# Kernel optimization log

Hardware: AMD Instinct MI355X
Metric: run time of the kernel (lower is better)

Reference implementation:

```python
import jax, jax.numpy as jnp
import numpy as np

B, S, D = 2, 2048, 2048
H, KVH, DH = 16, 4, 128
EPS = 1e-6
ROPE_BASE = 10000.0


def _rms_norm(x, eps=EPS):
    # weightless RMSNorm over the last (head) dim
    return x * jax.lax.rsqrt(jnp.mean(jnp.square(x), axis=-1, keepdims=True) + eps)


def _rope(x):
    # x: [b, s, h, d]; standard half-split RoPE, base 10000
    d = x.shape[-1]
    s = x.shape[1]
    inv_freq = 1.0 / (ROPE_BASE ** (jnp.arange(0, d // 2, dtype=jnp.float32) * 2.0 / d))
    ang = jnp.arange(s, dtype=jnp.float32)[:, None] * inv_freq[None, :]  # [s, d/2]
    cos = jnp.cos(ang)[None, :, None, :]
    sin = jnp.sin(ang)[None, :, None, :]
    x1, x2 = jnp.split(x, 2, axis=-1)
    return jnp.concatenate([x1 * cos - x2 * sin, x1 * sin + x2 * cos], axis=-1)


def setup_inputs() -> dict:
    key = jax.random.key(0)
    ks = jax.random.split(key, 5)
    x = jax.random.normal(ks[0], (B, S, D), dtype=jnp.float32)
    mask = jnp.tril(jnp.ones((S, S), dtype=bool))  # causal
    # eqx.Linear-style weights: [out, in], scaled init
    wq = jax.random.normal(ks[1], (D, D), dtype=jnp.float32) / np.sqrt(D)
    wk = jax.random.normal(ks[2], (KVH * DH, D), dtype=jnp.float32) / np.sqrt(D)
    wv = jax.random.normal(ks[3], (KVH * DH, D), dtype=jnp.float32) / np.sqrt(D)
    wo = jax.random.normal(ks[4], (D, D), dtype=jnp.float32) / np.sqrt(D)
    return {"x": x, "mask": mask, "wq": wq, "wk": wk, "wv": wv, "wo": wo}


def reference(x, mask, wq, wk, wv, wo):
    b, s, _ = x.shape
    q = jnp.einsum('bsi,oi->bso', x, wq).reshape(b, s, H, DH)
    k = jnp.einsum('bsi,oi->bso', x, wk).reshape(b, s, KVH, DH)
    v = jnp.einsum('bsi,oi->bso', x, wv).reshape(b, s, KVH, DH)
    rep = H // KVH
    k = jnp.repeat(k, rep, axis=-2)  # [b, s, H, DH]
    v = jnp.repeat(v, rep, axis=-2)
    q = _rms_norm(q)
    k = _rms_norm(k)
    q = _rope(q)
    k = _rope(k)
    scores = jnp.einsum('bshd,bthd->bhst', q, k) / jnp.sqrt(jnp.float32(DH))
    scores = jnp.where(mask[None, None], scores, -jnp.inf)
    w = jax.nn.softmax(scores, axis=-1)
    out = jnp.einsum('bhst,bthd->bshd', w, v).reshape(b, s, D)
    return jnp.einsum('bsi,oi->bso', out, wo)
```

## Files before the change

### kernel.cpp

```cpp
#include <hip/hip_runtime.h>
#include <hip/hip_bf16.h>

typedef unsigned short u16;
typedef unsigned int   u32;
typedef unsigned long long u64;
typedef __attribute__((ext_vector_type(8))) short bf16x8;
typedef __attribute__((ext_vector_type(4))) float f32x4;
typedef __attribute__((ext_vector_type(16))) float f32x16;

#define MFMA16(a,b,c) __builtin_amdgcn_mfma_f32_16x16x32_bf16((a),(b),(c),0,0,0)
#define MFMA32(a,b,c) __builtin_amdgcn_mfma_f32_32x32x16_bf16((a),(b),(c),0,0,0)

#define GLD16(gp, lp) __builtin_amdgcn_global_load_lds( \
    (const __attribute__((address_space(1))) void*)(gp), \
    (__attribute__((address_space(3))) void*)(lp), 16, 0, 0)

__device__ inline u32 pkbf(float a, float b) {
  __hip_bfloat16 ha = __float2bfloat16(a), hb = __float2bfloat16(b);
  return (u32)(*(u16*)&ha) | ((u32)(*(u16*)&hb) << 16);
}
__device__ inline float b2f(u16 x) {
  __hip_bfloat16 h; *(u16*)&h = x; return __bfloat162float(h);
}
__device__ inline u32 pk2(float a, float b) {
  u32 ua = __builtin_bit_cast(u32, a) + 0x8000u;
  u32 ub = __builtin_bit_cast(u32, b) + 0x8000u;
  return __builtin_amdgcn_perm(ub, ua, 0x07060302u);
}
__device__ inline float fmax3(float a, float b, float c) {
  return fmaxf(fmaxf(a, b), c);
}

__global__ __launch_bounds__(256) void cast_f32_bf16(const float* __restrict__ src,
                                                     u16* __restrict__ dst, int n4) {
  int i = blockIdx.x * 256 + threadIdx.x;
  if (i >= n4) return;
  float4 v = reinterpret_cast<const float4*>(src)[i];
  uint2 pk; pk.x = pkbf(v.x, v.y); pk.y = pkbf(v.z, v.w);
  reinterpret_cast<uint2*>(dst)[i] = pk;
}

__device__ inline void cstore(u16* C, size_t i, float v) {
  __hip_bfloat16 h = __float2bfloat16(v); C[i] = *(u16*)&h;
}
__device__ inline void cstore(float* C, size_t i, float v) { C[i] = v; }

template<typename OutT>
__global__ __launch_bounds__(512, 4) void gemm_big(const u16* __restrict__ A,
                                                   const u16* __restrict__ B,
                                                   OutT* __restrict__ C,
                                                   int M, int N, int K) {
  __shared__ u16 As[2][128 * 32];
  __shared__ u16 Bs[2][256 * 32];

  const int t = threadIdx.x;
  const int lane = t & 63, wid = t >> 6;
  const int l15 = lane & 15, l4 = lane >> 4;
  const int wr = wid >> 2, wc = wid & 3;

  const int nwg = gridDim.x * gridDim.y;
  int lid = blockIdx.y * gridDim.x + blockIdx.x;
  lid = (lid & 7) * (nwg >> 3) + (lid >> 3);
  const int m0 = (lid / gridDim.x) * 128, n0 = (lid % gridDim.x) * 256;

  const int ra = t >> 2;
  const int ca = (t & 3) ^ ((ra >> 1) & 3);
  const u16* Ag  = A + (size_t)(m0 + ra) * K + ca * 8;
  const u16* Bg0 = B + (size_t)(n0 + ra) * K + ca * 8;
  const u16* Bg1 = B + (size_t)(n0 + 128 + ra) * K + ca * 8;

#define STAGE(k0_, buf_) do {                                                 \
    GLD16(Ag  + (k0_), &As[buf_][t * 8]);                                     \
    GLD16(Bg0 + (k0_), &Bs[buf_][t * 8]);                                     \
    GLD16(Bg1 + (k0_), &Bs[buf_][4096 + t * 8]);                              \
  } while (0)

  const int nk = K >> 5;
  const int ks = (l15 >> 1) & 3;
  const int coff = ((l4 ^ ks) << 3);

  f32x4 acc[4][4] = {};

  STAGE(0, 0);
  STAGE(32, 1);

  for (int j = 0; j < nk; ++j) {
    const int cur = j & 1;
    if (j + 1 < nk) asm volatile("s_waitcnt vmcnt(3)" ::: "memory");
    else            asm volatile("s_waitcnt vmcnt(0)" ::: "memory");
    __builtin_amdgcn_s_barrier();
    __builtin_amdgcn_sched_barrier(0);

    bf16x8 af[4], bfr[4];
#pragma unroll
    for (int mi = 0; mi < 4; ++mi)
      af[mi] = *(const bf16x8*)&As[cur][(wr * 64 + mi * 16 + l15) * 32 + coff];
#pragma unroll
    for (int ni = 0; ni < 4; ++ni)
      bfr[ni] = *(const bf16x8*)&Bs[cur][(wc * 64 + ni * 16 + l15) * 32 + coff];
    __builtin_amdgcn_s_setprio(1);
#pragma unroll
    for (int mi = 0; mi < 4; ++mi)
#pragma unroll
      for (int ni = 0; ni < 4; ++ni)
        acc[mi][ni] = MFMA16(af[mi], bfr[ni], acc[mi][ni]);
    __builtin_amdgcn_s_setprio(0);

    __builtin_amdgcn_s_barrier();
    if (j + 2 < nk) STAGE((j + 2) << 5, cur);
  }

  const int crow = m0 + wr * 64 + (l4 << 2);
  const int ccol = n0 + wc * 64 + l15;
#pragma unroll
  for (int mi = 0; mi < 4; ++mi)
#pragma unroll
    for (int ni = 0; ni < 4; ++ni)
#pragma unroll
      for (int r = 0; r < 4; ++r)
        cstore(C, (size_t)(crow + mi * 16 + r) * N + (ccol + ni * 16), acc[mi][ni][r]);
#undef STAGE
}

__global__ __launch_bounds__(256) void rmsrope_kernel(u16* __restrict__ qkv) {
  const int t = threadIdx.x;
  const int lane = t & 63;
  const int gw = blockIdx.x * 4 + (t >> 6);
  const int row = gw / 20;
  const int hd = gw - row * 20;
  const int col = (hd < 16) ? hd * 128 : 2048 + (hd - 16) * 128;
  const size_t base = (size_t)row * 3072 + col;
  float x1 = b2f(qkv[base + lane]);
  float x2 = b2f(qkv[base + 64 + lane]);
  float ss = x1 * x1 + x2 * x2;
#pragma unroll
  for (int off = 32; off >= 1; off >>= 1) ss += __shfl_xor(ss, off, 64);
  const float qsc = (hd < 16) ? (0.08838834764831845f * 1.44269504088896340f)
                              : 1.0f;
  const float sc = rsqrtf(ss * (1.0f / 128.0f) + 1e-6f) * qsc;
  const int pos = row & 2047;
  const float inv_freq = exp2f(-(float)lane * (13.287712379549449f / 64.0f));
  float sn, cs;
  sincosf((float)pos * inv_freq, &sn, &cs);
  const float a = x1 * sc, b2 = x2 * sc;
  __hip_bfloat16 o1 = __float2bfloat16(a * cs - b2 * sn);
  __hip_bfloat16 o2 = __float2bfloat16(a * sn + b2 * cs);
  qkv[base + lane] = *(u16*)&o1;
  qkv[base + 64 + lane] = *(u16*)&o2;
}

__global__ __launch_bounds__(256) void vtrans_kernel(const u16* __restrict__ qkv,
                                                     u16* __restrict__ vt) {
  __shared__ u16 Ls[64 * 130];
  const int t = threadIdx.x;
  const int g = blockIdx.x & 7, sb = blockIdx.x >> 3;
  const int b = g >> 2, kvh = g & 3;
  const int vcol = 2560 + kvh * 128;
  {
    const int row = t >> 4, dch = t & 15;
    const u16* src = qkv + (size_t)(b * 2048 + sb * 64 + row) * 3072 + vcol + dch * 8;
#pragma unroll
    for (int it = 0; it < 4; ++it) {
      bf16x8 v = *(const bf16x8*)(src + (size_t)it * 16 * 3072);
      *(bf16x8*)&Ls[(row + it * 16) * 130 + dch * 8] = v;
    }
  }
  __syncthreads();
  const int c = t & 7, d0 = t >> 3;
  const int k0 = 4 * (8 * (c >> 2) + 4 * ((c >> 1) & 1) + (c & 1));
#pragma unroll
  for (int it = 0; it < 4; ++it) {
    const int d = d0 + 32 * it;
    u16 v[8];
#pragma unroll
    for (int e = 0; e < 8; ++e)
      v[e] = Ls[(k0 + (e & 3) + 8 * (e >> 2)) * 130 + d];
    u64 lo = (u64)v[0] | ((u64)v[1] << 16) | ((u64)v[2] << 32) | ((u64)v[3] << 48);
    u64 hi = (u64)v[4] | ((u64)v[5] << 16) | ((u64)v[6] << 32) | ((u64)v[7] << 48);
    u64* dst = (u64*)(vt + ((size_t)g * 128 + d) * 2048 + sb * 64 + c * 8);
    dst[0] = lo; dst[1] = hi;
  }
}

__global__ __launch_bounds__(256, 2) void attn_kernel(const u16* __restrict__ qkv,
                                                      const u16* __restrict__ vt,
                                                      u16* __restrict__ ao) {
  __shared__ u16 Ks[2][64 * 128];
  __shared__ u16 Vt[2][128 * 64];

  const int t = threadIdx.x;
  const int lane = t & 63, w = t >> 6;
  const int l31 = lane & 31, hi = lane >> 5;
  const int qg = w >> 1, hi2 = w & 1;

  const int bid = blockIdx.x;
  const int g = bid & 7;
  const int b = g >> 2, kvh = g & 3;
  const int idx = bid >> 3;
  const int h = kvh * 4 + (idx & 3);
  const int j = idx >> 2;

  const int kcol = 2048 + kvh * 128;
  const u16* vtg = vt + (size_t)g * 128 * 2048;

  const int krow_s = t >> 4, kchk = t & 15;
  const int vd = t >> 3, vc = t & 7;

#define STAGE_K(kb_, buf_) do {                                               \
    const size_t rb_ = (size_t)(b * 2048 + (kb_) * 64);                       \
    _Pragma("unroll")                                                         \
    for (int j_ = 0; j_ < 4; ++j_) {                                          \
      const int row_ = j_ * 16 + krow_s;                                      \
      GLD16(qkv + (rb_ + row_) * 3072 + kcol + ((kchk ^ (row_ & 7)) << 3),    \
            &Ks[buf_][(j_ * 256 + t) << 3]);                                  \
    } } while (0)

#define STAGE_V(kb_, buf_) do {                                               \
    _Pragma("unroll")                                                         \
    for (int j_ = 0; j_ < 4; ++j_) {                                          \
      const int d_ = j_ * 32 + vd;                                            \
      GLD16(vtg + (size_t)d_ * 2048 + (kb_) * 64 + ((vc ^ (d_ & 7)) << 3),    \
            &Vt[buf_][(j_ * 256 + t) << 3]);                                  \
    } } while (0)

  for (int ph = 0; ph < 2; ++ph) {
    const int qt64 = ph ? (31 - j) : j;
    const int q0 = qt64 * 64;
    const int nt = qt64 + 1;
    const int qrow = q0 + 32 * qg + l31;

    bf16x8 qf[8];
    {
      const u16* qp = qkv + (size_t)(b * 2048 + qrow) * 3072 + h * 128 + hi * 8;
#pragma unroll
      for (int st = 0; st < 8; ++st) qf[st] = *(const bf16x8*)(qp + st * 16);
    }

    f32x16 o[4];
#pragma unroll
    for (int dt = 0; dt < 4; ++dt)
#pragma unroll
      for (int i = 0; i < 16; ++i) o[dt][i] = 0.f;
    float m2 = -1e30f, l = 0.f;

    STAGE_K(0, 0);
    STAGE_V(0, 0);

    for (int kb = 0; kb < nt; ++kb) {
      const int cur = kb & 1;
      __syncthreads();
      const bool have_next = (kb + 1 < nt);
      if (have_next) {
        STAGE_K(kb + 1, cur ^ 1);
        STAGE_V(kb + 1, cur ^ 1);
      }

      f32x16 s;
#pragma unroll
      for (int i = 0; i < 16; ++i) s[i] = 0.f;
      const int kbase = (32 * hi2 + l31) * 128;
      const int ksw = l31 & 7;
      __builtin_amdgcn_s_setprio(1);
#pragma unroll
      for (int st = 0; st < 8; ++st) {
        bf16x8 ka = *(const bf16x8*)&Ks[cur][kbase + (((2 * st + hi) ^ ksw) << 3)];
        s = MFMA32(ka, qf[st], s);
      }
      __builtin_amdgcn_s_setprio(0);

      const bool nomask = (kb < qt64) || (hi2 == 0 && qg == 1);
      if (!nomask) {
#pragma unroll
        for (int i = 0; i < 16; ++i) {
          const int kr = kb * 64 + 32 * hi2 + (i & 3) + 8 * (i >> 2) + 4 * hi;
          s[i] = (kr <= qrow) ? s[i] : -INFINITY;
        }
      }
      float a0 = fmax3(s[0], s[1], s[2]);
      float a1 = fmax3(s[3], s[4], s[5]);
      float a2 = fmax3(s[6], s[7], s[8]);
      float a3 = fmax3(s[9], s[10], s[11]);
      float a4 = fmax3(s[12], s[13], s[14]);
      float b0 = fmax3(a0, a1, s[15]);
      float b1 = fmax3(a2, a3, a4);
      float pm = fmaxf(b0, b1);
      pm = fmaxf(pm, __shfl_xor(pm, 32));
      if (!__all(pm <= m2 + 8.f)) {
        const float m2n = fmaxf(m2, pm);
        const float fc = exp2f(m2 - m2n);
        m2 = m2n; l *= fc;
#pragma unroll
        for (int dt = 0; dt < 4; ++dt)
#pragma unroll
          for (int i = 0; i < 16; ++i) o[dt][i] *= fc;
      }
#pragma unroll
      for (int i = 0; i < 16; ++i) s[i] = exp2f(s[i] - m2);
      float t8[8];
#pragma unroll
      for (int i = 0; i < 8; ++i) t8[i] = s[i] + s[i + 8];
#pragma unroll
      for (int i = 0; i < 4; ++i) t8[i] = t8[i] + t8[i + 4];
      l += (t8[0] + t8[1]) + (t8[2] + t8[3]);
      union PB { u32 wd[4]; bf16x8 v; } p0u, p1u;
#pragma unroll
      for (int q_ = 0; q_ < 4; ++q_) {
        p0u.wd[q_] = pk2(s[2 * q_],     s[2 * q_ + 1]);
        p1u.wd[q_] = pk2(s[8 + 2 * q_], s[8 + 2 * q_ + 1]);
      }
      __builtin_amdgcn_s_setprio(1);
#pragma unroll
      for (int dt = 0; dt < 4; ++dt) {
        const int vrow = (dt * 32 + l31) * 64;
        const int dsw = l31 & 7;
        bf16x8 va0 = *(const bf16x8*)&Vt[cur][vrow + (((4 * hi2 + hi) ^ dsw) << 3)];
        o[dt] = MFMA32(va0, p0u.v, o[dt]);
        bf16x8 va1 = *(const bf16x8*)&Vt[cur][vrow + (((4 * hi2 + 2 + hi) ^ dsw) << 3)];
        o[dt] = MFMA32(va1, p1u.v, o[dt]);
      }
      __builtin_amdgcn_s_setprio(0);
    }

    __syncthreads();
    const float l_tot = l + __shfl_xor(l, 32);
    float* Mrg = (float*)&Ks[0][0];
    float* Mlb = (float*)&Vt[0][0];
    const int sw8 = l31 & 7;
    if (hi2) {
#pragma unroll
      for (int dt = 0; dt < 4; ++dt) {
        const int rbase = ((qg * 4 + dt) * 32 + l31) * 32;
#pragma unroll
        for (int m_ = 0; m_ < 4; ++m_) {
          f32x4 cv;
          cv[0] = o[dt][4 * m_ + 0]; cv[1] = o[dt][4 * m_ + 1];
          cv[2] = o[dt][4 * m_ + 2]; cv[3] = o[dt][4 * m_ + 3];
          *(f32x4*)&Mrg[rbase + (((hi * 4 + m_) ^ sw8) << 2)] = cv;
        }
      }
      if (hi == 0) {
        Mlb[qg * 64 + l31] = m2;
        Mlb[qg * 64 + 32 + l31] = l_tot;
      }
    }
    __syncthreads();
    if (!hi2) {
      const float m1 = Mlb[qg * 64 + l31];
      const float l1 = Mlb[qg * 64 + 32 + l31];
      const float ms = fmaxf(m2, m1);
      const float w0 = exp2f(m2 - ms), w1 = exp2f(m1 - ms);
      const float inv = 1.f / (w0 * l_tot + w1 * l1);
      const float aw0 = w0 * inv, aw1 = w1 * inv;
      const size_t orow = (size_t)(b * 2048 + qrow) * 2048 + h * 128;
#pragma unroll
      for (int dt = 0; dt < 4; ++dt) {
        const int rbase = ((qg * 4 + dt) * 32 + l31) * 32;
#pragma unroll
        for (int m_ = 0; m_ < 4; ++m_) {
          f32x4 o1v = *(const f32x4*)&Mrg[rbase + (((hi * 4 + m_) ^ sw8) << 2)];
          u64 val = 0;
#pragma unroll
          for (int r = 0; r < 4; ++r) {
            __hip_bfloat16 hb =
                __float2bfloat16(aw0 * o[dt][4 * m_ + r] + aw1 * o1v[r]);
            val |= (u64)(*(u16*)&hb) << (16 * r);
          }
          *(u64*)&ao[orow + dt * 32 + 8 * m_ + 4 * hi] = val;
        }
      }
    }
    __syncthreads();
  }
#undef STAGE_K
#undef STAGE_V
}

extern "C" void kernel_launch(void* const* d_in, const int* in_sizes, int n_in,
                              void* d_out, int out_size, void* d_ws, size_t ws_size,
                              hipStream_t stream) {
  const float* x  = (const float*)d_in[0];
  const float* wq = (const float*)d_in[2];
  const float* wk = (const float*)d_in[3];
  const float* wv = (const float*)d_in[4];
  const float* wo = (const float*)d_in[5];
  float* out = (float*)d_out;

  u16* xb   = (u16*)d_ws;
  u16* wqkv = xb + (size_t)8388608;
  u16* qkv  = wqkv + (size_t)6291456;
  u16* vtg  = qkv + (size_t)12582912;
  u16* ao   = xb;
  u16* wob  = wqkv;

  cast_f32_bf16<<<8192, 256, 0, stream>>>(x,  xb,   2097152);
  cast_f32_bf16<<<4096, 256, 0, stream>>>(wq, wqkv, 1048576);
  cast_f32_bf16<<<1024, 256, 0, stream>>>(wk, wqkv + (size_t)4194304, 262144);
  cast_f32_bf16<<<1024, 256, 0, stream>>>(wv, wqkv + (size_t)5242880, 262144);

  gemm_big<u16><<<dim3(12, 32), 512, 0, stream>>>(xb, wqkv, qkv, 4096, 3072, 2048);

  cast_f32_bf16<<<4096, 256, 0, stream>>>(wo, wob, 1048576);

  rmsrope_kernel<<<20480, 256, 0, stream>>>(qkv);
  vtrans_kernel<<<256, 256, 0, stream>>>(qkv, vtg);

  attn_kernel<<<512, 256, 0, stream>>>(qkv, vtg, ao);

  gemm_big<float><<<dim3(8, 32), 512, 0, stream>>>(ao, wob, out, 4096, 2048, 2048);
}
```

Baseline: 219.8 us.

## Enlarge attention query tile to 128 rows with 8 waves per block

Each attention block now handles 128 query rows with 512 threads instead of 64 rows with 256 threads, so every staged K/V tile in shared memory is reused by twice as many query rows. The launch grid is halved, causal pairing moves to 128-row tiles, and the mask test is recomputed per wave. Shared memory becomes one flat buffer sized for the larger merge scratch. The launch bound asks for more waves per execution unit, which halves the register budget and could cause spills. With only 256 blocks, parallelism per CU is also lower.

```diff
diff --git a/kernel.cpp b/kernel.cpp
--- a/kernel.cpp
+++ b/kernel.cpp
@@ -182,11 +182,12 @@
   }
 }
 
-__global__ __launch_bounds__(256, 2) void attn_kernel(const u16* __restrict__ qkv,
+__global__ __launch_bounds__(512, 4) void attn_kernel(const u16* __restrict__ qkv,
                                                       const u16* __restrict__ vt,
                                                       u16* __restrict__ ao) {
-  __shared__ u16 Ks[2][64 * 128];
-  __shared__ u16 Vt[2][128 * 64];
+  __shared__ u16 SM[33280];
+#define KS(buf) (&SM[(buf) * 8192])
+#define VT(buf) (&SM[16384 + (buf) * 8192])
 
   const int t = threadIdx.x;
   const int lane = t & 63, w = t >> 6;
@@ -198,7 +199,7 @@
   const int b = g >> 2, kvh = g & 3;
   const int idx = bid >> 3;
   const int h = kvh * 4 + (idx & 3);
-  const int j = idx >> 2;
+  const int J = idx >> 2;
 
   const int kcol = 2048 + kvh * 128;
   const u16* vtg = vt + (size_t)g * 128 * 2048;
@@ -209,25 +210,25 @@
 #define STAGE_K(kb_, buf_) do {                                               \
     const size_t rb_ = (size_t)(b * 2048 + (kb_) * 64);                       \
     _Pragma("unroll")                                                         \
-    for (int j_ = 0; j_ < 4; ++j_) {                                          \
-      const int row_ = j_ * 16 + krow_s;                                      \
+    for (int j_ = 0; j_ < 2; ++j_) {                                          \
+      const int row_ = j_ * 32 + krow_s;                                      \
       GLD16(qkv + (rb_ + row_) * 3072 + kcol + ((kchk ^ (row_ & 7)) << 3),    \
-            &Ks[buf_][(j_ * 256 + t) << 3]);                                  \
+            KS(buf_) + ((j_ * 512 + t) << 3));                                \
     } } while (0)
 
 #define STAGE_V(kb_, buf_) do {                                               \
     _Pragma("unroll")                                                         \
-    for (int j_ = 0; j_ < 4; ++j_) {                                          \
-      const int d_ = j_ * 32 + vd;                                            \
+    for (int j_ = 0; j_ < 2; ++j_) {                                          \
+      const int d_ = j_ * 64 + vd;                                            \
       GLD16(vtg + (size_t)d_ * 2048 + (kb_) * 64 + ((vc ^ (d_ & 7)) << 3),    \
-            &Vt[buf_][(j_ * 256 + t) << 3]);                                  \
+            VT(buf_) + ((j_ * 512 + t) << 3));                                \
     } } while (0)
 
   for (int ph = 0; ph < 2; ++ph) {
-    const int qt64 = ph ? (31 - j) : j;
-    const int q0 = qt64 * 64;
-    const int nt = qt64 + 1;
-    const int qrow = q0 + 32 * qg + l31;
+    const int qt = ph ? (15 - J) : J;
+    const int q0 = qt * 128;
+    const int nt = 2 * qt + 2;
+    const int qrow = q0 + qg * 32 + l31;
 
     bf16x8 qf[8];
     {
@@ -263,12 +264,12 @@
       __builtin_amdgcn_s_setprio(1);
 #pragma unroll
       for (int st = 0; st < 8; ++st) {
-        bf16x8 ka = *(const bf16x8*)&Ks[cur][kbase + (((2 * st + hi) ^ ksw) << 3)];
+        bf16x8 ka = *(const bf16x8*)&KS(cur)[kbase + (((2 * st + hi) ^ ksw) << 3)];
         s = MFMA32(ka, qf[st], s);
       }
       __builtin_amdgcn_s_setprio(0);
 
-      const bool nomask = (kb < qt64) || (hi2 == 0 && qg == 1);
+      const bool nomask = (kb * 64 + 32 * hi2 + 31) <= (q0 + qg * 32);
       if (!nomask) {
 #pragma unroll
         for (int i = 0; i < 16; ++i) {
@@ -313,9 +314,9 @@
       for (int dt = 0; dt < 4; ++dt) {
         const int vrow = (dt * 32 + l31) * 64;
         const int dsw = l31 & 7;
-        bf16x8 va0 = *(const bf16x8*)&Vt[cur][vrow + (((4 * hi2 + hi) ^ dsw) << 3)];
+        bf16x8 va0 = *(const bf16x8*)&VT(cur)[vrow + (((4 * hi2 + hi) ^ dsw) << 3)];
         o[dt] = MFMA32(va0, p0u.v, o[dt]);
-        bf16x8 va1 = *(const bf16x8*)&Vt[cur][vrow + (((4 * hi2 + 2 + hi) ^ dsw) << 3)];
+        bf16x8 va1 = *(const bf16x8*)&VT(cur)[vrow + (((4 * hi2 + 2 + hi) ^ dsw) << 3)];
         o[dt] = MFMA32(va1, p1u.v, o[dt]);
       }
       __builtin_amdgcn_s_setprio(0);
@@ -323,8 +324,8 @@
 
     __syncthreads();
     const float l_tot = l + __shfl_xor(l, 32);
-    float* Mrg = (float*)&Ks[0][0];
-    float* Mlb = (float*)&Vt[0][0];
+    float* Mrg = (float*)SM;
+    float* Mlb = (float*)&SM[32768];
     const int sw8 = l31 & 7;
     if (hi2) {
 #pragma unroll
@@ -373,6 +374,8 @@
   }
 #undef STAGE_K
 #undef STAGE_V
+#undef KS
+#undef VT
 }
 
 extern "C" void kernel_launch(void* const* d_in, const int* in_sizes, int n_in,
@@ -404,7 +407,7 @@
   rmsrope_kernel<<<20480, 256, 0, stream>>>(qkv);
   vtrans_kernel<<<256, 256, 0, stream>>>(qkv, vtg);
 
-  attn_kernel<<<512, 256, 0, stream>>>(qkv, vtg, ao);
+  attn_kernel<<<256, 512, 0, stream>>>(qkv, vtg, ao);
 
   gemm_big<float><<<dim3(8, 32), 512, 0, stream>>>(ao, wob, out, 4096, 2048, 2048);
 }
```

New measurement: 285.7 us. +30.0%, slower.
